# Performance work log

Measured on AMD Instinct MI355X. Metric: run time of the kernel, lower is better.

The kernel has to match this reference:

```python
import jax, jax.numpy as jnp
import numpy as np

B, S, D = 2, 4096, 1024
P_DROP = 0.2


def setup_inputs() -> dict:
    key = jax.random.key(0)
    ks = jax.random.split(key, 8)
    scale = 1.0 / np.sqrt(D)
    return {
        "x": jax.random.normal(ks[0], (B, S, D), jnp.float32),
        "Wq": jax.random.normal(ks[1], (D, D), jnp.float32) * scale,
        "bq": jnp.zeros((D,), jnp.float32),
        "Wk": jax.random.normal(ks[2], (D, D), jnp.float32) * scale,
        "bk": jnp.zeros((D,), jnp.float32),
        "Wv": jax.random.normal(ks[3], (D, D), jnp.float32) * scale,
        "bv": jnp.zeros((D,), jnp.float32),
        "dropout_u": jax.random.uniform(ks[4], (B, S, S), jnp.float32),
    }


def reference(x, Wq, bq, Wk, bk, Wv, bv, dropout_u):
    # torch nn.Linear: y = x @ W.T + b
    Q = jnp.einsum("bsd,ed->bse", x, Wq) + bq
    K = jnp.einsum("bsd,ed->bse", x, Wk) + bk
    V = jnp.einsum("bsd,ed->bse", x, Wv) + bv
    # NOTE: original has no 1/sqrt(d) scaling
    scores = jnp.einsum("bqd,bkd->bqk", Q, K)  # [B,S,S]
    attn = jax.nn.softmax(scores, axis=-1)
    # inverted dropout, p=0.2, deterministic mask from dropout_u
    mask = (dropout_u >= P_DROP).astype(attn.dtype) / (1.0 - P_DROP)
    attn = attn * mask
    return jnp.einsum("bqk,bkd->bqd", attn, V)
```

## Files before the change

kernel.cpp:

```cpp
#include <hip/hip_runtime.h>

typedef float    f32x4 __attribute__((ext_vector_type(4)));
typedef _Float16 f16x8 __attribute__((ext_vector_type(8)));
typedef _Float16 f16x4 __attribute__((ext_vector_type(4)));
typedef _Float16 f16;

#define DEVFN static __device__ __forceinline__

constexpr int BB = 2, SS = 4096, DD = 1024;
constexpr int MROWS = BB * SS;

constexpr size_t SZ_QK   = (size_t)MROWS * DD * 2;
constexpr size_t SZ_VT   = (size_t)BB * DD * SS * 2;
constexpr size_t SZ_ATTN = (size_t)BB * SS * SS * 2;
constexpr size_t SZ_S    = (size_t)BB * SS * SS * 4;
constexpr size_t SZ_W    = (size_t)DD * DD * 2;

constexpr size_t O_VT   = 0;
constexpr size_t O_ATTN = O_VT + SZ_VT;
constexpr size_t O_Q    = O_ATTN;
constexpr size_t O_K    = O_Q + 2 * SZ_QK;
constexpr size_t O_S    = O_ATTN + SZ_ATTN;
constexpr size_t O_XH   = O_S;
constexpr size_t O_WQH  = O_XH + SZ_QK;
constexpr size_t O_WKH  = O_WQH + SZ_W;
constexpr size_t O_WVH  = O_WKH + SZ_W;
constexpr size_t WS_NEEDED = SZ_VT + SZ_ATTN + SZ_S;

DEVFN f32x4 mfma16x16x32(f16x8 a, f16x8 b, f32x4 c) {
  return __builtin_amdgcn_mfma_f32_16x16x32_f16(a, b, c, 0, 0, 0);
}

DEVFN void gld16(const f16* g, char* l) {
  __builtin_amdgcn_global_load_lds((const __attribute__((address_space(1))) void*)g,
                                   (__attribute__((address_space(3))) void*)l, 16, 0, 0);
}

DEVFN void swz_xy(int& bx, int& by, int& bz) {
  const int gx = gridDim.x, gy = gridDim.y, gz = gridDim.z;
  const int lin = (blockIdx.z * gy + blockIdx.y) * gx + blockIdx.x;
  const int chunk = (gx * gy * gz) >> 3;
  const int nl = (lin & 7) * chunk + (lin >> 3);
  bx = nl % gx; const int r = nl / gx; by = r % gy; bz = r / gy;
}

DEVFN void gemm128_core(const f16* Ap, const f16* Bp, size_t ld, int NT,
                        char* smem, f32x4 (&acc)[4][4]) {
  const int tid = threadIdx.x, lane = tid & 63, wave = tid >> 6;
  const int wm = wave >> 1, wn = wave & 1;
  const size_t rk = (size_t)(tid >> 3) * ld +
                    (size_t)((((lane & 7) ^ (lane >> 3)) << 3));
  const int wvoff = wave << 10;
  const int rbA = (((wm << 6) + (lane & 15)) << 7);
  const int rbB = (((wn << 6) + (lane & 15)) << 7);
  const int cx0 = (((lane >> 4) << 4)) ^ ((lane & 7) << 4);
  const int cx1 = cx0 ^ 64;

  char* LA0 = smem;
  char* LA1 = smem + 32768;
  char* LA2 = smem + 65536;
  char* LB0 = smem + 98304;
  char* LB1 = smem + 114688;

  auto stA = [&](int u, int q, char* dst) {
    int uc = (u < NT) ? u : (NT - 1);
    gld16(Ap + (size_t)(q << 6) * ld + ((size_t)uc << 6) + rk, dst + (q << 13) + wvoff);
  };
  auto stB = [&](int u, int q, char* dst) {
    int uc = (u < NT) ? u : (NT - 1);
    gld16(Bp + (size_t)(q << 6) * ld + ((size_t)uc << 6) + rk, dst + (q << 13) + wvoff);
  };
  auto rdA = [&](char* l, int m, int cx) { return *(const f16x8*)(l + rbA + (m << 11) + cx); };
  auto rdB = [&](char* l, int n, int cx) { return *(const f16x8*)(l + rbB + (n << 11) + cx); };

  f16x8 A0[2][2], B0[2][2], A0n[2][2], B0n[2][2];

  stA(0, 0, LA0); stA(0, 1, LA0); stA(0, 2, LA0); stA(0, 3, LA0);
  stB(0, 0, LB0); stB(0, 1, LB0);
  stA(1, 0, LA1); stA(1, 1, LA1); stA(1, 2, LA1); stA(1, 3, LA1);
  stB(1, 0, LB1); stB(1, 1, LB1);
  asm volatile("s_waitcnt vmcnt(6)" ::: "memory");
  __builtin_amdgcn_s_barrier();
#pragma unroll
  for (int n = 0; n < 2; ++n) { B0[n][0] = rdB(LB0, n, cx0); B0[n][1] = rdB(LB0, n, cx1); }
#pragma unroll
  for (int m = 0; m < 2; ++m) { A0[m][0] = rdA(LA0, m, cx0); A0[m][1] = rdA(LA0, m, cx1); }

  char *aC = LA0, *aN = LA1, *aN2 = LA2, *bC = LB0, *bN = LB1;

  auto tileX = [&](char* lA, char* lB, char* lAn, char* lA2, char* lBn, int t,
                   f16x8 (&a0)[2][2], f16x8 (&b0)[2][2],
                   f16x8 (&a0n)[2][2], f16x8 (&b0n)[2][2]) {
    f16x8 a1[2][2], b1[2][2];
#pragma unroll
    for (int n = 0; n < 2; ++n) { b1[n][0] = rdB(lB, n + 2, cx0); b1[n][1] = rdB(lB, n + 2, cx1); }
    stA(t + 2, 0, lA2); stA(t + 2, 1, lA2);
    __builtin_amdgcn_s_barrier();
    asm volatile("s_waitcnt lgkmcnt(4)" ::: "memory");
    __builtin_amdgcn_sched_barrier(0);
    __builtin_amdgcn_s_setprio(1);
#pragma unroll
    for (int m = 0; m < 2; ++m)
#pragma unroll
      for (int n = 0; n < 2; ++n) {
        acc[m][n] = mfma16x16x32(a0[m][0], b0[n][0], acc[m][n]);
        acc[m][n] = mfma16x16x32(a0[m][1], b0[n][1], acc[m][n]);
      }
    __builtin_amdgcn_s_setprio(0);
    __builtin_amdgcn_s_barrier();
#pragma unroll
    for (int m = 0; m < 2; ++m) { a1[m][0] = rdA(lA, m + 2, cx0); a1[m][1] = rdA(lA, m + 2, cx1); }
    stA(t + 2, 2, lA2); stA(t + 2, 3, lA2);
    asm volatile("s_waitcnt vmcnt(4)" ::: "memory");
    __builtin_amdgcn_s_barrier();
    asm volatile("s_waitcnt lgkmcnt(4)" ::: "memory");
    __builtin_amdgcn_sched_barrier(0);
    __builtin_amdgcn_s_setprio(1);
#pragma unroll
    for (int m = 0; m < 2; ++m)
#pragma unroll
      for (int n = 0; n < 2; ++n) {
        acc[m][n + 2] = mfma16x16x32(a0[m][0], b1[n][0], acc[m][n + 2]);
        acc[m][n + 2] = mfma16x16x32(a0[m][1], b1[n][1], acc[m][n + 2]);
      }
    __builtin_amdgcn_s_setprio(0);
    __builtin_amdgcn_s_barrier();
#pragma unroll
    for (int n = 0; n < 2; ++n) { b0n[n][0] = rdB(lBn, n, cx0); b0n[n][1] = rdB(lBn, n, cx1); }
    stB(t + 2, 0, lB); stB(t + 2, 1, lB);
    __builtin_amdgcn_s_barrier();
    asm volatile("s_waitcnt lgkmcnt(4)" ::: "memory");
    __builtin_amdgcn_sched_barrier(0);
    __builtin_amdgcn_s_setprio(1);
#pragma unroll
    for (int m = 0; m < 2; ++m)
#pragma unroll
      for (int n = 0; n < 2; ++n) {
        acc[m + 2][n] = mfma16x16x32(a1[m][0], b0[n][0], acc[m + 2][n]);
        acc[m + 2][n] = mfma16x16x32(a1[m][1], b0[n][1], acc[m + 2][n]);
      }
    __builtin_amdgcn_s_setprio(0);
    __builtin_amdgcn_s_barrier();
#pragma unroll
    for (int m = 0; m < 2; ++m) { a0n[m][0] = rdA(lAn, m, cx0); a0n[m][1] = rdA(lAn, m, cx1); }
    __builtin_amdgcn_s_barrier();
    asm volatile("s_waitcnt lgkmcnt(4)" ::: "memory");
    __builtin_amdgcn_sched_barrier(0);
    __builtin_amdgcn_s_setprio(1);
#pragma unroll
    for (int m = 0; m < 2; ++m)
#pragma unroll
      for (int n = 0; n < 2; ++n) {
        acc[m + 2][n + 2] = mfma16x16x32(a1[m][0], b1[n][0], acc[m + 2][n + 2]);
        acc[m + 2][n + 2] = mfma16x16x32(a1[m][1], b1[n][1], acc[m + 2][n + 2]);
      }
    __builtin_amdgcn_s_setprio(0);
    __builtin_amdgcn_s_barrier();
  };

  for (int t = 0; t < NT; t += 2) {
    tileX(aC, bC, aN, aN2, bN, t, A0, B0, A0n, B0n);
    { char* tmp = aC; aC = aN; aN = aN2; aN2 = tmp; }
    { char* tmp = bC; bC = bN; bN = tmp; }
    tileX(aC, bC, aN, aN2, bN, t + 1, A0n, B0n, A0, B0);
    { char* tmp = aC; aC = aN; aN = aN2; aN2 = tmp; }
    { char* tmp = bC; bC = bN; bN = tmp; }
  }
  asm volatile("s_waitcnt vmcnt(0)" ::: "memory");
}

__global__ __launch_bounds__(512, 2)
void gemm_sc128(const f16* __restrict__ Q, const f16* __restrict__ Kp,
                float* __restrict__ Sf) {
  extern __shared__ char smem[];
  const int lin = (blockIdx.z * 16 + blockIdx.y) * 32 + blockIdx.x;
  const int g = (lin & 7) * 128 + (lin >> 3);
  const int bz = g >> 9;
  const int w = g & 511;
  const int t = w >> 7, s = w & 127;
  const int bx = (t & 1) * 16 + (s & 15);
  const int by = (t >> 1) * 8 + (s >> 4);
  const size_t zo = (size_t)bz * SS * DD;
  const int row0 = by * 256, col0 = bx * 128;
  f32x4 acc[4][4] = {};
  gemm128_core(Q + zo + (size_t)row0 * DD, Kp + zo + (size_t)col0 * DD,
               DD, 16, smem, acc);

  float* C = Sf + (size_t)bz * SS * SS;
  const int lane = threadIdx.x & 63, wave = threadIdx.x >> 6;
  const int wm = wave >> 1, wn = wave & 1;
#pragma unroll
  for (int m = 0; m < 4; ++m)
#pragma unroll
    for (int n = 0; n < 4; ++n) {
      int col = col0 + wn * 64 + n * 16 + (lane & 15);
      int rowb = row0 + wm * 64 + m * 16 + (lane >> 4) * 4;
#pragma unroll
      for (int j = 0; j < 4; ++j)
        C[(size_t)(rowb + j) * SS + col] = acc[m][n][j];
    }
}

__global__ __launch_bounds__(512, 2)
void gemm_projvt128(const f16* __restrict__ xh,
                    const f16* __restrict__ wqh, const f16* __restrict__ wkh,
                    const f16* __restrict__ wvh,
                    const float* __restrict__ bq, const float* __restrict__ bk,
                    const float* __restrict__ bvv,
                    f16* __restrict__ Q, f16* __restrict__ K,
                    f16* __restrict__ Vt) {
  extern __shared__ char smem[];
  const int lin = blockIdx.x;
  const int id = (lin & 7) * 96 + (lin >> 3);
  const int lane = threadIdx.x & 63, wave = threadIdx.x >> 6;
  const int wm = wave >> 1, wn = wave & 1;
  f32x4 acc[4][4] = {};

  if (id < 512) {
    const int bx = id & 15, by = id >> 4;
    const int row0 = by * 256;
    const bool isK = bx >= 8;
    const int col0 = (bx & 7) * 128;
    const f16* B0p = isK ? wkh : wqh;
    const float* bias = isK ? bk : bq;
    f16* CH = isK ? K : Q;
    gemm128_core(xh + (size_t)row0 * DD, B0p + (size_t)col0 * DD, DD, 16, smem, acc);
#pragma unroll
    for (int m = 0; m < 4; ++m)
#pragma unroll
      for (int n = 0; n < 4; ++n) {
        int col = col0 + wn * 64 + n * 16 + (lane & 15);
        float bvv2 = bias[col];
        int rowb = row0 + wm * 64 + m * 16 + (lane >> 4) * 4;
#pragma unroll
        for (int j = 0; j < 4; ++j)
          CH[(size_t)(rowb + j) * DD + col] = (f16)(acc[m][n][j] + bvv2);
      }
  } else {
    const int id2 = id - 512;
    const int bx = id2 & 63, by = id2 >> 6;
    const int row0 = by * 256, col0 = bx * 128;
    gemm128_core(wvh + (size_t)row0 * DD, xh + (size_t)col0 * DD, DD, 16, smem, acc);
#pragma unroll
    for (int m = 0; m < 4; ++m)
#pragma unroll
      for (int n = 0; n < 4; ++n) {
        int col = col0 + wn * 64 + n * 16 + (lane & 15);
        int batch = col >> 12, sl = col & 4095;
        int rowb = row0 + wm * 64 + m * 16 + (lane >> 4) * 4;
#pragma unroll
        for (int j = 0; j < 4; ++j) {
          float v = acc[m][n][j] + bvv[rowb + j];
          Vt[(size_t)batch * DD * SS + (size_t)(rowb + j) * SS + sl] = (f16)v;
        }
      }
  }
}

__global__ __launch_bounds__(512, 2)
void gemm_pv128(const f16* __restrict__ Pb, const f16* __restrict__ Vt,
                float* __restrict__ out) {
  extern __shared__ char smem[];
  int bx, by, bz; swz_xy(bx, by, bz);
  const int row0 = by * 256;
  const int col0 = bx * 128;
  f32x4 acc[4][4] = {};
  gemm128_core(Pb + (size_t)bz * SS * SS + (size_t)row0 * SS,
               Vt + (size_t)bz * DD * SS + (size_t)col0 * SS,
               SS, 64, smem, acc);

  float* C = out + (size_t)bz * SS * DD;
  const int lane = threadIdx.x & 63, wave = threadIdx.x >> 6;
  const int wm = wave >> 1, wn = wave & 1;
#pragma unroll
  for (int m = 0; m < 4; ++m)
#pragma unroll
    for (int n = 0; n < 4; ++n) {
      int col = col0 + wn * 64 + n * 16 + (lane & 15);
      int rowb = row0 + wm * 64 + m * 16 + (lane >> 4) * 4;
#pragma unroll
      for (int j = 0; j < 4; ++j)
        __builtin_nontemporal_store(acc[m][n][j], &C[(size_t)(rowb + j) * DD + col]);
    }
}

__global__ __launch_bounds__(256)
void split_all(const float* __restrict__ x, const float* __restrict__ Wq,
               const float* __restrict__ Wk, const float* __restrict__ Wv,
               f16* __restrict__ xh, f16* __restrict__ wqh,
               f16* __restrict__ wkh, f16* __restrict__ wvh) {
  const int b = blockIdx.x, tid = threadIdx.x;
  const float* in; f16* hi; int nv, rb, nb;
  if (b < 1536)      { in = x;  hi = xh;  nv = (MROWS * DD) >> 2; rb = b;        nb = 1536; }
  else if (b < 1792) { in = Wq; hi = wqh; nv = (DD * DD) >> 2;    rb = b - 1536; nb = 256; }
  else if (b < 2048) { in = Wk; hi = wkh; nv = (DD * DD) >> 2;    rb = b - 1792; nb = 256; }
  else               { in = Wv; hi = wvh; nv = (DD * DD) >> 2;    rb = b - 2048; nb = 256; }
  for (int i = rb * 256 + tid; i < nv; i += nb * 256) {
    f32x4 v = *(const f32x4*)(in + (size_t)i * 4);
    f16x4 h;
#pragma unroll
    for (int e = 0; e < 4; ++e) h[e] = (f16)v[e];
    *(f16x4*)(hi + (size_t)i * 4) = h;
  }
}

__global__ __launch_bounds__(256)
void softmax_dropout(const float* __restrict__ Sf, const float* __restrict__ U,
                     f16* __restrict__ P) {
  __shared__ float red[4];
  const size_t row = blockIdx.x;
  const float* s = Sf + row * SS;
  const float* u = U + row * SS;
  f16* p = P + row * SS;
  const int tid = threadIdx.x, lane = tid & 63, wave = tid >> 6;

  f32x4 v[4];
  float m = -3.0e38f;
#pragma unroll
  for (int j = 0; j < 4; ++j) {
    v[j] = __builtin_nontemporal_load((const f32x4*)(s + (size_t)(j * 256 + tid) * 4));
#pragma unroll
    for (int e = 0; e < 4; ++e) m = fmaxf(m, v[j][e]);
  }
#pragma unroll
  for (int o = 32; o > 0; o >>= 1) m = fmaxf(m, __shfl_xor(m, o));
  if (lane == 0) red[wave] = m;
  __syncthreads();
  m = fmaxf(fmaxf(red[0], red[1]), fmaxf(red[2], red[3]));

  float sum = 0.0f;
#pragma unroll
  for (int j = 0; j < 4; ++j)
#pragma unroll
    for (int e = 0; e < 4; ++e) { float ex = __expf(v[j][e] - m); v[j][e] = ex; sum += ex; }
#pragma unroll
  for (int o = 32; o > 0; o >>= 1) sum += __shfl_xor(sum, o);
  __syncthreads();
  if (lane == 0) red[wave] = sum;
  __syncthreads();
  sum = red[0] + red[1] + red[2] + red[3];
  const float scale = 1.25f / sum;

#pragma unroll
  for (int j = 0; j < 4; ++j) {
    f32x4 uu = __builtin_nontemporal_load((const f32x4*)(u + (size_t)(j * 256 + tid) * 4));
    f16x4 out;
#pragma unroll
    for (int e = 0; e < 4; ++e)
      out[e] = (f16)((uu[e] >= 0.2f) ? v[j][e] * scale : 0.0f);
    *(f16x4*)(p + (size_t)(j * 256 + tid) * 4) = out;
  }
}

extern "C" void kernel_launch(void* const* d_in, const int* in_sizes, int n_in,
                              void* d_out, int out_size, void* d_ws, size_t ws_size,
                              hipStream_t stream) {
  if (ws_size < WS_NEEDED) return;

  const float* x  = (const float*)d_in[0];
  const float* Wq = (const float*)d_in[1];
  const float* bq = (const float*)d_in[2];
  const float* Wk = (const float*)d_in[3];
  const float* bk = (const float*)d_in[4];
  const float* Wv = (const float*)d_in[5];
  const float* bv = (const float*)d_in[6];
  const float* du = (const float*)d_in[7];

  char* ws = (char*)d_ws;
  f16*   Vt  = (f16*)(ws + O_VT);
  f16*   Pb  = (f16*)(ws + O_ATTN);
  f16*   Q   = (f16*)(ws + O_Q);
  f16*   K   = (f16*)(ws + O_K);
  float* Sf  = (float*)(ws + O_S);
  f16*   xh  = (f16*)(ws + O_XH);
  f16*   wqh = (f16*)(ws + O_WQH);
  f16*   wkh = (f16*)(ws + O_WKH);
  f16*   wvh = (f16*)(ws + O_WVH);
  float* out = (float*)d_out;

  hipFuncSetAttribute((const void*)gemm_sc128,
                      hipFuncAttributeMaxDynamicSharedMemorySize, 131072);
  hipFuncSetAttribute((const void*)gemm_projvt128,
                      hipFuncAttributeMaxDynamicSharedMemorySize, 131072);
  hipFuncSetAttribute((const void*)gemm_pv128,
                      hipFuncAttributeMaxDynamicSharedMemorySize, 131072);

  split_all<<<2304, 256, 0, stream>>>(x, Wq, Wk, Wv, xh, wqh, wkh, wvh);

  gemm_projvt128<<<768, 512, 131072, stream>>>(
      xh, wqh, wkh, wvh, bq, bk, bv, Q, K, Vt);

  gemm_sc128<<<dim3(32, 16, BB), 512, 131072, stream>>>(Q, K, Sf);

  softmax_dropout<<<MROWS, 256, 0, stream>>>(Sf, du, Pb);

  gemm_pv128<<<dim3(DD / 128, SS / 256, BB), 512, 131072, stream>>>(Pb, Vt, out);
}
```

Measured before the change: 258.8 us.

## Enlarge QK^T score GEMM tile to 256x256 with new pipelined core

Replaces the 256x128-tile score GEMM with a 256x256-tile kernel built on a new core that triple-buffers A and double-buffers B in 80 KB of LDS. Each wave now computes a 128x64 sub-tile, which raises arithmetic intensity and halves the number of workgroups and redundant Q/K loads. The cost is more accumulator registers per thread (128 fp32), which could hurt occupancy or cause spills. The grid swizzle is reworked to match, and the lower LDS use could let more blocks fit per CU.

```diff
diff --git a/kernel.cpp b/kernel.cpp
--- a/kernel.cpp
+++ b/kernel.cpp
@@ -169,32 +169,115 @@
   asm volatile("s_waitcnt vmcnt(0)" ::: "memory");
 }
 
+DEVFN void gemm256sq_core(const f16* Ap, const f16* Bp, size_t ld, int NT,
+                          char* smem, f32x4 (&acc)[8][4]) {
+  const int tid = threadIdx.x, lane = tid & 63, wave = tid >> 6;
+  const int wm = wave >> 2, wn = wave & 3;
+  const size_t rk = (size_t)(tid >> 2) * ld +
+                    (size_t)((((tid & 3) ^ ((tid >> 2) & 3)) << 3));
+  const int wvoff = wave << 10;
+  const int rbA = (wm << 13) + ((lane & 15) << 6);
+  const int rbB = (wn << 12) + ((lane & 15) << 6);
+  const int csw = (((lane >> 4) ^ (lane & 3)) << 4);
+
+  char* A0b = smem;
+  char* A1b = smem + 16384;
+  char* A2b = smem + 32768;
+  char* B0b = smem + 49152;
+  char* B1b = smem + 65536;
+
+  auto stA = [&](int u, int c, char* dst) {
+    int uc = (u < NT) ? u : (NT - 1);
+    gld16(Ap + (size_t)(c << 7) * ld + (uc << 5) + rk, dst + (c << 13) + wvoff);
+  };
+  auto stB = [&](int u, int c, char* dst) {
+    int uc = (u < NT) ? u : (NT - 1);
+    gld16(Bp + (size_t)(c << 7) * ld + (uc << 5) + rk, dst + (c << 13) + wvoff);
+  };
+  auto rdA = [&](char* buf, int half, int f) {
+    return *(const f16x8*)(buf + rbA + (half << 12) + (f << 10) + csw);
+  };
+  auto rdB = [&](char* buf, int f) {
+    return *(const f16x8*)(buf + rbB + (f << 10) + csw);
+  };
+
+  f16x8 a0[4], a1[4], b[4], a0n[4], bn[4];
+
+  stA(0, 0, A0b); stA(0, 1, A0b);
+  stB(0, 0, B0b); stB(0, 1, B0b);
+  stA(1, 0, A1b); stA(1, 1, A1b);
+  stB(1, 0, B1b); stB(1, 1, B1b);
+  asm volatile("s_waitcnt vmcnt(4)" ::: "memory");
+  __builtin_amdgcn_s_barrier();
+#pragma unroll
+  for (int f = 0; f < 4; ++f) a0[f] = rdA(A0b, 0, f);
+#pragma unroll
+  for (int f = 0; f < 4; ++f) b[f] = rdB(B0b, f);
+
+  for (int t = 0; t < NT; ++t) {
+#pragma unroll
+    for (int f = 0; f < 4; ++f) a1[f] = rdA(A0b, 1, f);
+    stA(t + 2, 0, A2b); stA(t + 2, 1, A2b);
+    asm volatile("s_waitcnt lgkmcnt(4)" ::: "memory");
+    __builtin_amdgcn_sched_barrier(0);
+    __builtin_amdgcn_s_setprio(1);
+#pragma unroll
+    for (int m = 0; m < 4; ++m)
+#pragma unroll
+      for (int n = 0; n < 4; ++n)
+        acc[m][n] = mfma16x16x32(a0[m], b[n], acc[m][n]);
+    __builtin_amdgcn_s_setprio(0);
+    asm volatile("s_waitcnt vmcnt(2)" ::: "memory");
+    __builtin_amdgcn_s_barrier();
+#pragma unroll
+    for (int f = 0; f < 4; ++f) bn[f] = rdB(B1b, f);
+#pragma unroll
+    for (int f = 0; f < 4; ++f) a0n[f] = rdA(A1b, 0, f);
+    stB(t + 2, 0, B0b); stB(t + 2, 1, B0b);
+    asm volatile("s_waitcnt lgkmcnt(8)" ::: "memory");
+    __builtin_amdgcn_sched_barrier(0);
+    __builtin_amdgcn_s_setprio(1);
+#pragma unroll
+    for (int m = 0; m < 4; ++m)
+#pragma unroll
+      for (int n = 0; n < 4; ++n)
+        acc[m + 4][n] = mfma16x16x32(a1[m], b[n], acc[m + 4][n]);
+    __builtin_amdgcn_s_setprio(0);
+    __builtin_amdgcn_s_barrier();
+    { char* tmp = A0b; A0b = A1b; A1b = A2b; A2b = tmp; }
+    { char* tmp = B0b; B0b = B1b; B1b = tmp; }
+#pragma unroll
+    for (int f = 0; f < 4; ++f) { a0[f] = a0n[f]; b[f] = bn[f]; }
+  }
+  asm volatile("s_waitcnt vmcnt(0)" ::: "memory");
+}
+
 __global__ __launch_bounds__(512, 2)
-void gemm_sc128(const f16* __restrict__ Q, const f16* __restrict__ Kp,
+void gemm_sc256(const f16* __restrict__ Q, const f16* __restrict__ Kp,
                 float* __restrict__ Sf) {
   extern __shared__ char smem[];
-  const int lin = (blockIdx.z * 16 + blockIdx.y) * 32 + blockIdx.x;
-  const int g = (lin & 7) * 128 + (lin >> 3);
-  const int bz = g >> 9;
-  const int w = g & 511;
-  const int t = w >> 7, s = w & 127;
-  const int bx = (t & 1) * 16 + (s & 15);
-  const int by = (t >> 1) * 8 + (s >> 4);
+  const int lin = (blockIdx.z * 16 + blockIdx.y) * 16 + blockIdx.x;
+  const int g = (lin & 7) * 64 + (lin >> 3);
+  const int bz = g >> 8;
+  const int w = g & 255;
+  const int st = w >> 6, s = w & 63;
+  const int bx = (st & 1) * 8 + (s & 7);
+  const int by = (st >> 1) * 8 + (s >> 3);
   const size_t zo = (size_t)bz * SS * DD;
-  const int row0 = by * 256, col0 = bx * 128;
-  f32x4 acc[4][4] = {};
-  gemm128_core(Q + zo + (size_t)row0 * DD, Kp + zo + (size_t)col0 * DD,
-               DD, 16, smem, acc);
+  const int row0 = by * 256, col0 = bx * 256;
+  f32x4 acc[8][4] = {};
+  gemm256sq_core(Q + zo + (size_t)row0 * DD, Kp + zo + (size_t)col0 * DD,
+                 DD, 32, smem, acc);
 
   float* C = Sf + (size_t)bz * SS * SS;
   const int lane = threadIdx.x & 63, wave = threadIdx.x >> 6;
-  const int wm = wave >> 1, wn = wave & 1;
-#pragma unroll
-  for (int m = 0; m < 4; ++m)
+  const int wm = wave >> 2, wn = wave & 3;
+#pragma unroll
+  for (int m = 0; m < 8; ++m)
 #pragma unroll
     for (int n = 0; n < 4; ++n) {
       int col = col0 + wn * 64 + n * 16 + (lane & 15);
-      int rowb = row0 + wm * 64 + m * 16 + (lane >> 4) * 4;
+      int rowb = row0 + wm * 128 + (m >> 2) * 64 + (m & 3) * 16 + (lane >> 4) * 4;
 #pragma unroll
       for (int j = 0; j < 4; ++j)
         C[(size_t)(rowb + j) * SS + col] = acc[m][n][j];
@@ -378,8 +461,8 @@
   f16*   wvh = (f16*)(ws + O_WVH);
   float* out = (float*)d_out;
 
-  hipFuncSetAttribute((const void*)gemm_sc128,
-                      hipFuncAttributeMaxDynamicSharedMemorySize, 131072);
+  hipFuncSetAttribute((const void*)gemm_sc256,
+                      hipFuncAttributeMaxDynamicSharedMemorySize, 81920);
   hipFuncSetAttribute((const void*)gemm_projvt128,
                       hipFuncAttributeMaxDynamicSharedMemorySize, 131072);
   hipFuncSetAttribute((const void*)gemm_pv128,
@@ -390,7 +473,7 @@
   gemm_projvt128<<<768, 512, 131072, stream>>>(
       xh, wqh, wkh, wvh, bq, bk, bv, Q, K, Vt);
 
-  gemm_sc128<<<dim3(32, 16, BB), 512, 131072, stream>>>(Q, K, Sf);
+  gemm_sc256<<<dim3(16, 16, BB), 512, 81920, stream>>>(Q, K, Sf);
 
   softmax_dropout<<<MROWS, 256, 0, stream>>>(Sf, du, Pb);
 
```

Measured after the change: 257.7 us. Within noise of the previous version (-0.4%).
